# Optimization experiments

Measured on AMD Instinct MI355X. Metric: run time of the kernel, lower is better.

Reference implementation:

```python
import jax, jax.numpy as jnp
import numpy as np

B, L, D, V = 64, 512, 768, 100
LN_EPS = 1e-6


def setup_inputs() -> dict:
    key = jax.random.key(0)
    k1, k2, k3, k4 = jax.random.split(key, 4)
    return {
        "ids": jax.random.randint(k1, (B, 1), 0, V),
        "pooler": jax.random.normal(k2, (B, L, D), dtype=jnp.float32),
        "emb_table": jax.random.normal(k3, (V, 2), dtype=jnp.float32),
        "W_dense": jax.random.normal(k4, (2, D), dtype=jnp.float32) * 0.1,
        "b_dense": jnp.zeros((D,), dtype=jnp.float32),
        "gamma": jnp.ones((D,), dtype=jnp.float32),
        "beta": jnp.zeros((D,), dtype=jnp.float32),
    }


def reference(ids, pooler, emb_table, W_dense, b_dense, gamma, beta):
    # id -> 2-dim projection -> dense to embed_dim: xt (B, 1, D)
    emb = emb_table[ids]                      # (B, 1, 2)
    xt = emb @ W_dense + b_dense              # (B, 1, D)

    # Per timestep i the original concatenates [pooler[:, i], xt] into a
    # 2-token sequence and runs dot-product self-attention (keras Attention,
    # no scaling), then sums over the 2 tokens. Vectorized over all L steps:
    tok = jnp.stack([pooler, jnp.broadcast_to(xt, pooler.shape)], axis=2)  # (B, L, 2, D)
    scores = jnp.einsum('blqd,blkd->blqk', tok, tok)                       # (B, L, 2, 2)
    attn = jax.nn.softmax(scores, axis=-1)
    out = jnp.einsum('blqk,blkd->blqd', attn, tok)                         # (B, L, 2, D)
    summed = out.sum(axis=2)                                               # (B, L, D)

    # dropout is identity at inference; layernorm over last axis, eps=1e-6
    mean = summed.mean(axis=-1, keepdims=True)
    var = summed.var(axis=-1, keepdims=True)
    normed = (summed - mean) * jax.lax.rsqrt(var + LN_EPS)
    return normed * gamma + beta
```

## Files before the change

kernel.cpp:

```cpp
#include <hip/hip_runtime.h>


constexpr int Bc = 64;
constexpr int Lc = 512;
constexpr int Dc = 768;
constexpr float LN_EPS = 1e-6f;
constexpr int WAVES_PER_BLOCK = 4;

typedef float nv_float4 __attribute__((ext_vector_type(4)));

__global__ __launch_bounds__(64 * WAVES_PER_BLOCK) void hier_attn_ln_kernel(
    const int*   __restrict__ ids,
    const float* __restrict__ pooler,
    const float* __restrict__ emb_table,
    const float* __restrict__ W,
    const float* __restrict__ bvec,
    const float* __restrict__ gamma,
    const float* __restrict__ beta,
    float*       __restrict__ out)
{
    const int wave = threadIdx.x >> 6;
    const int lane = threadIdx.x & 63;
    const int row  = blockIdx.x * WAVES_PER_BLOCK + wave;
    const int b    = row >> 9;

    const float4* prow4 = (const float4*)(pooler + (size_t)row * Dc);
    nv_float4*    orow4 = (nv_float4*)(out + (size_t)row * Dc);
    const float4* W0_4  = (const float4*)W;
    const float4* W1_4  = (const float4*)(W + Dc);
    const float4* b_4   = (const float4*)bvec;
    const float4* g_4   = (const float4*)gamma;
    const float4* be_4  = (const float4*)beta;

    const int id = ids[b];
    const float e0 = emb_table[id * 2 + 0];
    const float e1 = emb_table[id * 2 + 1];

    float4 t0[3], t1[3];
    float s00 = 0.f, s01 = 0.f, s11 = 0.f, S0 = 0.f, S1 = 0.f;

#pragma unroll
    for (int j = 0; j < 3; ++j) {
        const int idx4 = lane + j * 64;
        float4 p  = prow4[idx4];
        float4 w0 = W0_4[idx4];
        float4 w1 = W1_4[idx4];
        float4 bd = b_4[idx4];
        float4 x;
        x.x = fmaf(e0, w0.x, fmaf(e1, w1.x, bd.x));
        x.y = fmaf(e0, w0.y, fmaf(e1, w1.y, bd.y));
        x.z = fmaf(e0, w0.z, fmaf(e1, w1.z, bd.z));
        x.w = fmaf(e0, w0.w, fmaf(e1, w1.w, bd.w));
        t0[j] = p;
        t1[j] = x;
        s00 += p.x*p.x + p.y*p.y + p.z*p.z + p.w*p.w;
        s01 += p.x*x.x + p.y*x.y + p.z*x.z + p.w*x.w;
        s11 += x.x*x.x + x.y*x.y + x.z*x.z + x.w*x.w;
        S0  += p.x + p.y + p.z + p.w;
        S1  += x.x + x.y + x.z + x.w;
    }

#pragma unroll
    for (int off = 32; off > 0; off >>= 1) {
        s00 += __shfl_xor(s00, off);
        s01 += __shfl_xor(s01, off);
        s11 += __shfl_xor(s11, off);
        S0  += __shfl_xor(S0,  off);
        S1  += __shfl_xor(S1,  off);
    }

    const float m0  = fmaxf(s00, s01);
    const float a00 = __expf(s00 - m0);
    const float a01 = __expf(s01 - m0);
    const float r0  = 1.f / (a00 + a01);
    const float m1  = fmaxf(s01, s11);
    const float a10 = __expf(s01 - m1);
    const float a11 = __expf(s11 - m1);
    const float r1  = 1.f / (a10 + a11);
    const float w0s = a00 * r0 + a10 * r1;
    const float w1s = a01 * r0 + a11 * r1;

    const float invD = 1.f / (float)Dc;
    const float mean = (w0s * S0 + w1s * S1) * invD;
    const float ex2  = (w0s*w0s*s00 + 2.f*w0s*w1s*s01 + w1s*w1s*s11) * invD;
    const float var  = ex2 - mean * mean;
    const float rstd = rsqrtf(var + LN_EPS);

#pragma unroll
    for (int j = 0; j < 3; ++j) {
        const int idx4 = lane + j * 64;
        float4 gm = g_4[idx4];
        float4 bt = be_4[idx4];
        nv_float4 o;
        o.x = (fmaf(w0s, t0[j].x, w1s * t1[j].x) - mean) * rstd * gm.x + bt.x;
        o.y = (fmaf(w0s, t0[j].y, w1s * t1[j].y) - mean) * rstd * gm.y + bt.y;
        o.z = (fmaf(w0s, t0[j].z, w1s * t1[j].z) - mean) * rstd * gm.z + bt.z;
        o.w = (fmaf(w0s, t0[j].w, w1s * t1[j].w) - mean) * rstd * gm.w + bt.w;
        __builtin_nontemporal_store(o, &orow4[idx4]);
    }
}

extern "C" void kernel_launch(void* const* d_in, const int* in_sizes, int n_in,
                              void* d_out, int out_size, void* d_ws, size_t ws_size,
                              hipStream_t stream) {
    const int*   ids       = (const int*)  d_in[0];
    const float* pooler    = (const float*)d_in[1];
    const float* emb_table = (const float*)d_in[2];
    const float* W_dense   = (const float*)d_in[3];
    const float* b_dense   = (const float*)d_in[4];
    const float* gamma     = (const float*)d_in[5];
    const float* beta      = (const float*)d_in[6];
    float* out = (float*)d_out;

    const int nrows = Bc * Lc;
    hipLaunchKernelGGL(hier_attn_ln_kernel,
                       dim3(nrows / WAVES_PER_BLOCK), dim3(64 * WAVES_PER_BLOCK),
                       0, stream,
                       ids, pooler, emb_table, W_dense, b_dense, gamma, beta, out);
}
```

Baseline: 187.3 us.

## Process four rows per wave and hoist per-batch projection and LN params

Each wave now handles four consecutive rows instead of one. The xt projection, its self-dot and sum reductions, and the gamma/beta loads are computed once per wave and reused across those rows. The output epilogue is folded into fused FMAs with rstd pre-multiplied into the attention weights. This removes redundant loads, FMAs and shuffle reductions per row, but it lowers the number of blocks and serializes the rows within a wave, which may reduce memory-level parallelism.

```diff
diff --git a/kernel.cpp b/kernel.cpp
--- a/kernel.cpp
+++ b/kernel.cpp
@@ -6,6 +6,8 @@
 constexpr int Dc = 768;
 constexpr float LN_EPS = 1e-6f;
 constexpr int WAVES_PER_BLOCK = 4;
+constexpr int ROWS_PER_WAVE   = 4;
+constexpr int ROWS_PER_BLOCK  = WAVES_PER_BLOCK * ROWS_PER_WAVE;
 
 typedef float nv_float4 __attribute__((ext_vector_type(4)));
 
@@ -21,82 +23,99 @@
 {
     const int wave = threadIdx.x >> 6;
     const int lane = threadIdx.x & 63;
-    const int row  = blockIdx.x * WAVES_PER_BLOCK + wave;
-    const int b    = row >> 9;
+    const int row0 = blockIdx.x * ROWS_PER_BLOCK + wave * ROWS_PER_WAVE;
+    const int b    = row0 >> 9;
 
-    const float4* prow4 = (const float4*)(pooler + (size_t)row * Dc);
-    nv_float4*    orow4 = (nv_float4*)(out + (size_t)row * Dc);
-    const float4* W0_4  = (const float4*)W;
-    const float4* W1_4  = (const float4*)(W + Dc);
-    const float4* b_4   = (const float4*)bvec;
-    const float4* g_4   = (const float4*)gamma;
-    const float4* be_4  = (const float4*)beta;
+    const float4* W0_4 = (const float4*)W;
+    const float4* W1_4 = (const float4*)(W + Dc);
+    const float4* b_4  = (const float4*)bvec;
+    const float4* g_4  = (const float4*)gamma;
+    const float4* be_4 = (const float4*)beta;
 
     const int id = ids[b];
     const float e0 = emb_table[id * 2 + 0];
     const float e1 = emb_table[id * 2 + 1];
 
-    float4 t0[3], t1[3];
-    float s00 = 0.f, s01 = 0.f, s11 = 0.f, S0 = 0.f, S1 = 0.f;
-
+    float4 xt[3], gm[3], bt[3];
+    float s11 = 0.f, S1 = 0.f;
 #pragma unroll
     for (int j = 0; j < 3; ++j) {
         const int idx4 = lane + j * 64;
-        float4 p  = prow4[idx4];
         float4 w0 = W0_4[idx4];
         float4 w1 = W1_4[idx4];
         float4 bd = b_4[idx4];
+        gm[j] = g_4[idx4];
+        bt[j] = be_4[idx4];
         float4 x;
         x.x = fmaf(e0, w0.x, fmaf(e1, w1.x, bd.x));
         x.y = fmaf(e0, w0.y, fmaf(e1, w1.y, bd.y));
         x.z = fmaf(e0, w0.z, fmaf(e1, w1.z, bd.z));
         x.w = fmaf(e0, w0.w, fmaf(e1, w1.w, bd.w));
-        t0[j] = p;
-        t1[j] = x;
-        s00 += p.x*p.x + p.y*p.y + p.z*p.z + p.w*p.w;
-        s01 += p.x*x.x + p.y*x.y + p.z*x.z + p.w*x.w;
+        xt[j] = x;
         s11 += x.x*x.x + x.y*x.y + x.z*x.z + x.w*x.w;
-        S0  += p.x + p.y + p.z + p.w;
         S1  += x.x + x.y + x.z + x.w;
     }
-
 #pragma unroll
     for (int off = 32; off > 0; off >>= 1) {
-        s00 += __shfl_xor(s00, off);
-        s01 += __shfl_xor(s01, off);
         s11 += __shfl_xor(s11, off);
-        S0  += __shfl_xor(S0,  off);
         S1  += __shfl_xor(S1,  off);
     }
 
-    const float m0  = fmaxf(s00, s01);
-    const float a00 = __expf(s00 - m0);
-    const float a01 = __expf(s01 - m0);
-    const float r0  = 1.f / (a00 + a01);
-    const float m1  = fmaxf(s01, s11);
-    const float a10 = __expf(s01 - m1);
-    const float a11 = __expf(s11 - m1);
-    const float r1  = 1.f / (a10 + a11);
-    const float w0s = a00 * r0 + a10 * r1;
-    const float w1s = a01 * r0 + a11 * r1;
-
     const float invD = 1.f / (float)Dc;
-    const float mean = (w0s * S0 + w1s * S1) * invD;
-    const float ex2  = (w0s*w0s*s00 + 2.f*w0s*w1s*s01 + w1s*w1s*s11) * invD;
-    const float var  = ex2 - mean * mean;
-    const float rstd = rsqrtf(var + LN_EPS);
+    const float4* p_base = (const float4*)(pooler + (size_t)row0 * Dc);
+    nv_float4*    o_base = (nv_float4*)(out + (size_t)row0 * Dc);
 
 #pragma unroll
-    for (int j = 0; j < 3; ++j) {
-        const int idx4 = lane + j * 64;
-        float4 gm = g_4[idx4];
-        float4 bt = be_4[idx4];
-        nv_float4 o;
-        o.x = (fmaf(w0s, t0[j].x, w1s * t1[j].x) - mean) * rstd * gm.x + bt.x;
-        o.y = (fmaf(w0s, t0[j].y, w1s * t1[j].y) - mean) * rstd * gm.y + bt.y;
-        o.z = (fmaf(w0s, t0[j].z, w1s * t1[j].z) - mean) * rstd * gm.z + bt.z;
-        o.w = (fmaf(w0s, t0[j].w, w1s * t1[j].w) - mean) * rstd * gm.w + bt.w;
-        __builtin_nontemporal_store(o, &orow4[idx4]);
+    for (int r = 0; r < ROWS_PER_WAVE; ++r) {
+        const float4* prow4 = p_base + (size_t)r * (Dc / 4);
+        nv_float4*    orow4 = o_base + (size_t)r * (Dc / 4);
+
+        float4 t0[3];
+        float s00 = 0.f, s01 = 0.f, S0 = 0.f;
+#pragma unroll
+        for (int j = 0; j < 3; ++j) {
+            float4 p = prow4[lane + j * 64];
+            t0[j] = p;
+            s00 += p.x*p.x + p.y*p.y + p.z*p.z + p.w*p.w;
+            s01 += p.x*xt[j].x + p.y*xt[j].y + p.z*xt[j].z + p.w*xt[j].w;
+            S0  += p.x + p.y + p.z + p.w;
+        }
+#pragma unroll
+        for (int off = 32; off > 0; off >>= 1) {
+            s00 += __shfl_xor(s00, off);
+            s01 += __shfl_xor(s01, off);
+            S0  += __shfl_xor(S0,  off);
+        }
+
+        const float m0  = fmaxf(s00, s01);
+        const float a00 = __expf(s00 - m0);
+        const float a01 = __expf(s01 - m0);
+        const float r0  = 1.f / (a00 + a01);
+        const float m1  = fmaxf(s01, s11);
+        const float a10 = __expf(s01 - m1);
+        const float a11 = __expf(s11 - m1);
+        const float r1  = 1.f / (a10 + a11);
+        const float w0s = a00 * r0 + a10 * r1;
+        const float w1s = a01 * r0 + a11 * r1;
+
+        const float mean = (w0s * S0 + w1s * S1) * invD;
+        const float ex2  = (w0s*w0s*s00 + 2.f*w0s*w1s*s01 + w1s*w1s*s11) * invD;
+        const float var  = ex2 - mean * mean;
+        const float rstd = rsqrtf(var + LN_EPS);
+
+        const float a = w0s * rstd;
+        const float c = w1s * rstd;
+        const float m = mean * rstd;
+
+#pragma unroll
+        for (int j = 0; j < 3; ++j) {
+            nv_float4 o;
+            o.x = fmaf(gm[j].x, fmaf(a, t0[j].x, fmaf(c, xt[j].x, -m)), bt[j].x);
+            o.y = fmaf(gm[j].y, fmaf(a, t0[j].y, fmaf(c, xt[j].y, -m)), bt[j].y);
+            o.z = fmaf(gm[j].z, fmaf(a, t0[j].z, fmaf(c, xt[j].z, -m)), bt[j].z);
+            o.w = fmaf(gm[j].w, fmaf(a, t0[j].w, fmaf(c, xt[j].w, -m)), bt[j].w);
+            __builtin_nontemporal_store(o, &orow4[lane + j * 64]);
+        }
     }
 }
 
@@ -114,7 +133,7 @@
 
     const int nrows = Bc * Lc;
     hipLaunchKernelGGL(hier_attn_ln_kernel,
-                       dim3(nrows / WAVES_PER_BLOCK), dim3(64 * WAVES_PER_BLOCK),
+                       dim3(nrows / ROWS_PER_BLOCK), dim3(64 * WAVES_PER_BLOCK),
                        0, stream,
                        ids, pooler, emb_table, W_dense, b_dense, gamma, beta, out);
 }
```

Result: slower. 193.9 us (+3.6%).
